# Kernel tuning notes

Hardware: AMD Instinct MI355X
Metric: run time of the kernel (lower is better)

## Reference

```python
import jax, jax.numpy as jnp
import numpy as np

B, S, D = 2, 4096, 256
H, DH, DM = 8, 32, 1024
ROPE_BASE = 10000.0
LN_EPS = 1e-5


def _layer_norm(x, g, b):
    mu = jnp.mean(x, axis=-1, keepdims=True)
    var = jnp.mean(jnp.square(x - mu), axis=-1, keepdims=True)
    return (x - mu) * jax.lax.rsqrt(var + LN_EPS) * g + b


def _rope(x):
    # x: [b, s, h, d_head]; lucidrains interleaved-pair RoPE
    s, d = x.shape[1], x.shape[-1]
    inv_freq = 1.0 / (ROPE_BASE ** (jnp.arange(0, d, 2, dtype=jnp.float32) / d))  # [d/2]
    freqs = jnp.arange(s, dtype=jnp.float32)[:, None] * inv_freq[None, :]          # [s, d/2]
    freqs = jnp.repeat(freqs, 2, axis=-1)                                          # [s, d]
    cos = jnp.cos(freqs)[None, :, None, :]
    sin = jnp.sin(freqs)[None, :, None, :]
    x1, x2 = x[..., 0::2], x[..., 1::2]
    rot = jnp.stack((-x2, x1), axis=-1).reshape(x.shape)
    return x * cos + rot * sin


def setup_inputs() -> dict:
    key = jax.random.key(0)
    ks = jax.random.split(key, 8)
    sw = 1.0 / np.sqrt(D)
    return {
        "x": jax.random.normal(ks[0], (B, S, D), jnp.float32),
        "Wq": jax.random.normal(ks[1], (D, D), jnp.float32) * sw,
        "Wk": jax.random.normal(ks[2], (D, D), jnp.float32) * sw,
        "Wv": jax.random.normal(ks[3], (D, D), jnp.float32) * sw,
        "Wo": jax.random.normal(ks[4], (D, D), jnp.float32) * sw,
        "ln1_g": jnp.ones((D,), jnp.float32),
        "ln1_b": jnp.zeros((D,), jnp.float32),
        "ln2_g": jnp.ones((D,), jnp.float32),
        "ln2_b": jnp.zeros((D,), jnp.float32),
        "W2": jax.random.normal(ks[5], (DM, D), jnp.float32) * sw,
        "b2": jnp.zeros((DM,), jnp.float32),
        "W3": jax.random.normal(ks[6], (D, DM), jnp.float32) * (1.0 / np.sqrt(DM)),
        "b3": jnp.zeros((D,), jnp.float32),
    }


def reference(x, Wq, Wk, Wv, Wo, ln1_g, ln1_b, ln2_g, ln2_b, W2, b2, W3, b3):
    b, s, d = x.shape
    h, dh = H, DH
    xn = _layer_norm(x, ln1_g, ln1_b)
    q = (xn @ Wq.T).reshape(b, s, h, dh)
    k = (xn @ Wk.T).reshape(b, s, h, dh)
    v = (xn @ Wv.T).reshape(b, s, h, dh)
    q = _rope(q)
    k = _rope(k)
    # scores: [b, h, q, k] (full matrix, matching original implementation)
    scores = jnp.einsum('bqhd,bkhd->bhqk', q, k) / np.sqrt(dh)
    attn = jax.nn.softmax(scores, axis=-1)
    out = jnp.einsum('bhqk,bkhd->bqhd', attn, v).reshape(b, s, d)
    out = out @ Wo.T
    mlp_in = out + x
    y = _layer_norm(mlp_in, ln2_g, ln2_b)
    y = jax.nn.gelu(y @ W2.T + b2, approximate=False)
    y = y @ W3.T + b3
    return y + mlp_in
```

## Files before the change

kernel.cpp:

```cpp
#include <hip/hip_runtime.h>
#include <math.h>

#define D 256
#define S 4096
#define H 8
#define DH 32
#define DM 1024
#define NTOK 8192

typedef __attribute__((ext_vector_type(8))) short short8;
typedef __attribute__((ext_vector_type(4))) float f32x4;

#define QSCALE (0.17677669529663687f * 1.4426950408889634f)

__device__ inline unsigned short f2bf(float f) {
    union { float f; unsigned u; } v; v.f = f;
    unsigned r = v.u + 0x7fffu + ((v.u >> 16) & 1u);
    return (unsigned short)(r >> 16);
}
__device__ inline void gload16(const void* g, void* l) {
    __builtin_amdgcn_global_load_lds((const __attribute__((address_space(1))) void*)g,
                                     (__attribute__((address_space(3))) void*)l, 16, 0, 0);
}

__device__ inline short8 pack_p(f32x4 s0, f32x4 s1) {
    unsigned u0[4], u1[4];
    #pragma unroll
    for (int i = 0; i < 4; ++i) {
        union { float f; unsigned u; } c0, c1;
        c0.f = __builtin_amdgcn_exp2f(s0[i]);
        c1.f = __builtin_amdgcn_exp2f(s1[i]);
        u0[i] = c0.u;
        u1[i] = c1.u;
    }
    union { unsigned u[4]; short8 s; } pk;
    pk.u[0] = __builtin_amdgcn_perm(u0[1], u0[0], 0x07060302u);
    pk.u[1] = __builtin_amdgcn_perm(u0[3], u0[2], 0x07060302u);
    pk.u[2] = __builtin_amdgcn_perm(u1[1], u1[0], 0x07060302u);
    pk.u[3] = __builtin_amdgcn_perm(u1[3], u1[2], 0x07060302u);
    return pk.s;
}

__global__ void prep(const float* __restrict__ Wq, const float* __restrict__ Wk,
                     const float* __restrict__ Wv, const float* __restrict__ Wo,
                     const float* __restrict__ W2, const float* __restrict__ W3,
                     unsigned short* __restrict__ wqkv, unsigned short* __restrict__ wo_b,
                     unsigned short* __restrict__ w2_b, unsigned short* __restrict__ w3_b,
                     float* __restrict__ ct, float* __restrict__ st,
                     const float* __restrict__ x, const float* __restrict__ g,
                     const float* __restrict__ b, unsigned short* __restrict__ xn) {
    int blk = blockIdx.x;
    if (blk < 3328) {
        int i = blk * 256 + threadIdx.x;
        if (i < 196608) {
            const float* s = (i < 65536) ? Wq : ((i < 131072) ? Wk : Wv);
            wqkv[i] = f2bf(s[i & 65535]);
        } else if (i < 262144) {
            wo_b[i - 196608] = f2bf(Wo[i - 196608]);
        } else if (i < 524288) {
            w2_b[i - 262144] = f2bf(W2[i - 262144]);
        } else if (i < 786432) {
            w3_b[i - 524288] = f2bf(W3[i - 524288]);
        } else {
            int j = i - 786432;
            int spos = j >> 4, pi = j & 15;
            float inv_freq = powf(10000.0f, -(float)(2 * pi) / 32.0f);
            float fr = (float)spos * inv_freq;
            ct[j] = cosf(fr);
            st[j] = sinf(fr);
        }
        return;
    }
    int l = threadIdx.x & 63;
    int row = (blk - 3328) * 4 + (threadIdx.x >> 6);
    const float4 v = *(const float4*)(x + (size_t)row * D + l * 4);
    float s  = v.x + v.y + v.z + v.w;
    float s2 = v.x * v.x + v.y * v.y + v.z * v.z + v.w * v.w;
    #pragma unroll
    for (int off = 32; off > 0; off >>= 1) {
        s  += __shfl_xor(s, off, 64);
        s2 += __shfl_xor(s2, off, 64);
    }
    float mu  = s * (1.0f / D);
    float var = s2 * (1.0f / D) - mu * mu;
    float rs  = rsqrtf(var + 1e-5f);
    const float4 gg = *(const float4*)(g + l * 4);
    const float4 bb = *(const float4*)(b + l * 4);
    ushort4 o;
    o.x = f2bf((v.x - mu) * rs * gg.x + bb.x);
    o.y = f2bf((v.y - mu) * rs * gg.y + bb.y);
    o.z = f2bf((v.z - mu) * rs * gg.z + bb.z);
    o.w = f2bf((v.w - mu) * rs * gg.w + bb.w);
    *(ushort4*)(xn + (size_t)row * D + l * 4) = o;
}

__global__ void ln_kernel(const float* __restrict__ x, const float* __restrict__ g,
                          const float* __restrict__ b, unsigned short* __restrict__ out) {
    int l = threadIdx.x & 63;
    int row = blockIdx.x * 4 + (threadIdx.x >> 6);
    const float4 v = *(const float4*)(x + (size_t)row * D + l * 4);
    float s  = v.x + v.y + v.z + v.w;
    float s2 = v.x * v.x + v.y * v.y + v.z * v.z + v.w * v.w;
    #pragma unroll
    for (int off = 32; off > 0; off >>= 1) {
        s  += __shfl_xor(s, off, 64);
        s2 += __shfl_xor(s2, off, 64);
    }
    float mu  = s * (1.0f / D);
    float var = s2 * (1.0f / D) - mu * mu;
    float rs  = rsqrtf(var + 1e-5f);
    const float4 gg = *(const float4*)(g + l * 4);
    const float4 bb = *(const float4*)(b + l * 4);
    ushort4 o;
    o.x = f2bf((v.x - mu) * rs * gg.x + bb.x);
    o.y = f2bf((v.y - mu) * rs * gg.y + bb.y);
    o.z = f2bf((v.z - mu) * rs * gg.z + bb.z);
    o.w = f2bf((v.w - mu) * rs * gg.w + bb.w);
    *(ushort4*)(out + (size_t)row * D + l * 4) = o;
}

__global__ __launch_bounds__(256) void gemm64b(const unsigned short* __restrict__ A,
        const unsigned short* __restrict__ Bw, void* __restrict__ outp,
        unsigned short* __restrict__ vt,
        const float* __restrict__ bias,
        const float* __restrict__ ct, const float* __restrict__ st,
        int N, int K, int mode) {
    __shared__ unsigned short As[2][64 * 64];
    __shared__ unsigned short Bs[2][64 * 64];
    int tid = threadIdx.x;
    int w = tid >> 6, l = tid & 63;
    int lm = l & 15, lg = l >> 4;
    int wm = (w >> 1) * 32, wn = (w & 1) * 32;
    int bm = blockIdx.x * 64, bn = blockIdx.y * 64;
    int r1 = tid >> 3, pc = tid & 7;
    int pcx = (pc ^ (r1 & 7)) * 8;
    const unsigned short* Ag1 = A + (size_t)(bm + r1) * K + pcx;
    const unsigned short* Ag2 = A + (size_t)(bm + 32 + r1) * K + pcx;
    const unsigned short* Bg1 = Bw + (size_t)(bn + r1) * K + pcx;
    const unsigned short* Bg2 = Bw + (size_t)(bn + 32 + r1) * K + pcx;
    const int swz = lm & 7;
    f32x4 acc[2][2] = {};

    gload16(Ag1, &As[0][w * 512]);
    gload16(Ag2, &As[0][2048 + w * 512]);
    gload16(Bg1, &Bs[0][w * 512]);
    gload16(Bg2, &Bs[0][2048 + w * 512]);
    for (int k0 = 0; k0 < K; k0 += 64) {
        int cur = (k0 >> 6) & 1;
        __syncthreads();
        if (k0 + 64 < K) {
            gload16(Ag1 + k0 + 64, &As[1 - cur][w * 512]);
            gload16(Ag2 + k0 + 64, &As[1 - cur][2048 + w * 512]);
            gload16(Bg1 + k0 + 64, &Bs[1 - cur][w * 512]);
            gload16(Bg2 + k0 + 64, &Bs[1 - cur][2048 + w * 512]);
        }
        #pragma unroll
        for (int j = 0; j < 2; ++j) {
            int ch = ((j * 4 + lg) ^ swz) * 8;
            short8 af[2], bf[2];
            #pragma unroll
            for (int i = 0; i < 2; ++i) af[i] = *(const short8*)&As[cur][(wm + i * 16 + lm) * 64 + ch];
            #pragma unroll
            for (int i = 0; i < 2; ++i) bf[i] = *(const short8*)&Bs[cur][(wn + i * 16 + lm) * 64 + ch];
            #pragma unroll
            for (int mi = 0; mi < 2; ++mi)
                #pragma unroll
                for (int ni = 0; ni < 2; ++ni)
                    acc[mi][ni] = __builtin_amdgcn_mfma_f32_16x16x32_bf16(af[mi], bf[ni], acc[mi][ni], 0, 0, 0);
        }
    }

    if (mode == 0) {
        if (bn >= 512) {
            #pragma unroll
            for (int mi = 0; mi < 2; ++mi) {
                #pragma unroll
                for (int ni = 0; ni < 2; ++ni) {
                    int ng = bn + wn + ni * 16 + lm - 512;
                    int hh = ng >> 5, dh = ng & 31;
                    int mg0 = bm + wm + mi * 16 + lg * 4;
                    int bb = mg0 >> 12, ss = mg0 & 4095;
                    ushort4 pv;
                    pv.x = f2bf(acc[mi][ni][0]); pv.y = f2bf(acc[mi][ni][1]);
                    pv.z = f2bf(acc[mi][ni][2]); pv.w = f2bf(acc[mi][ni][3]);
                    *(ushort4*)(vt + ((size_t)((bb * 8 + hh) * 32 + dh)) * S + ss) = pv;
                }
            }
        } else {
            #pragma unroll
            for (int mi = 0; mi < 2; ++mi) {
                #pragma unroll
                for (int ni = 0; ni < 2; ++ni) {
                    int ng = bn + wn + ni * 16 + lm;
                    int pi = (ng & 31) >> 1;
                    float sgn = (ng & 1) ? 1.f : -1.f;
                    float qs  = (ng < 256) ? QSCALE : 1.f;
                    #pragma unroll
                    for (int r2 = 0; r2 < 4; ++r2) {
                        int mg = bm + wm + mi * 16 + lg * 4 + r2;
                        int spos = mg & (S - 1);
                        float vv = acc[mi][ni][r2];
                        float pv = __shfl_xor(vv, 1, 64);
                        float cs = ct[spos * 16 + pi];
                        float sn = st[spos * 16 + pi];
                        float ov = (vv * cs + sgn * pv * sn) * qs;
                        ((unsigned short*)outp)[(size_t)mg * N + ng] = f2bf(ov);
                    }
                }
            }
        }
        return;
    }
    #pragma unroll
    for (int mi = 0; mi < 2; ++mi) {
        #pragma unroll
        for (int ni = 0; ni < 2; ++ni) {
            int ng = bn + wn + ni * 16 + lm;
            #pragma unroll
            for (int r2 = 0; r2 < 4; ++r2) {
                int mg = bm + wm + mi * 16 + lg * 4 + r2;
                float t = acc[mi][ni][r2] + bias[ng];
                ((unsigned short*)outp)[(size_t)mg * N + ng] =
                    f2bf(0.5f * t * (1.0f + erff(t * 0.70710678118654752f)));
            }
        }
    }
}

__global__ __launch_bounds__(256) void gemm32(const unsigned short* __restrict__ A,
        const unsigned short* __restrict__ Bw, void* __restrict__ outp,
        const float* __restrict__ bias, const float* __restrict__ res,
        int N, int K, int mode) {
    __shared__ unsigned short As[2][32 * 128];
    __shared__ unsigned short Bs[2][64 * 128];
    int tid = threadIdx.x;
    int w = tid >> 6, l = tid & 63;
    int lm = l & 15, lg = l >> 4;
    int rm = (w >> 1) * 16, wn = (w & 1) * 32;
    int bm = blockIdx.x * 32, bn = blockIdx.y * 64;
    int r1 = tid >> 4, pc = tid & 15;
    int pcx = (pc ^ (r1 & 7)) * 8;
    const unsigned short* Ag1 = A + (size_t)(bm + r1) * K + pcx;
    const unsigned short* Ag2 = A + (size_t)(bm + 16 + r1) * K + pcx;
    const unsigned short* Bg1 = Bw + (size_t)(bn + r1) * K + pcx;
    const unsigned short* Bg2 = Bw + (size_t)(bn + 16 + r1) * K + pcx;
    const unsigned short* Bg3 = Bw + (size_t)(bn + 32 + r1) * K + pcx;
    const unsigned short* Bg4 = Bw + (size_t)(bn + 48 + r1) * K + pcx;
    const int swz = lm & 7;
    f32x4 acc[2] = {};

    gload16(Ag1, &As[0][w * 512]);
    gload16(Ag2, &As[0][2048 + w * 512]);
    gload16(Bg1, &Bs[0][w * 512]);
    gload16(Bg2, &Bs[0][2048 + w * 512]);
    gload16(Bg3, &Bs[0][4096 + w * 512]);
    gload16(Bg4, &Bs[0][6144 + w * 512]);
    for (int k0 = 0; k0 < K; k0 += 128) {
        int cur = (k0 >> 7) & 1;
        __syncthreads();
        if (k0 + 128 < K) {
            gload16(Ag1 + k0 + 128, &As[1 - cur][w * 512]);
            gload16(Ag2 + k0 + 128, &As[1 - cur][2048 + w * 512]);
            gload16(Bg1 + k0 + 128, &Bs[1 - cur][w * 512]);
            gload16(Bg2 + k0 + 128, &Bs[1 - cur][2048 + w * 512]);
            gload16(Bg3 + k0 + 128, &Bs[1 - cur][4096 + w * 512]);
            gload16(Bg4 + k0 + 128, &Bs[1 - cur][6144 + w * 512]);
        }
        #pragma unroll
        for (int j = 0; j < 4; ++j) {
            int ch = ((j * 4 + lg) ^ swz) * 8;
            short8 af = *(const short8*)&As[cur][(rm + lm) * 128 + ch];
            short8 bf[2];
            #pragma unroll
            for (int i = 0; i < 2; ++i) bf[i] = *(const short8*)&Bs[cur][(wn + i * 16 + lm) * 128 + ch];
            #pragma unroll
            for (int ni = 0; ni < 2; ++ni)
                acc[ni] = __builtin_amdgcn_mfma_f32_16x16x32_bf16(af, bf[ni], acc[ni], 0, 0, 0);
        }
    }

    #pragma unroll
    for (int ni = 0; ni < 2; ++ni) {
        int ng = bn + wn + ni * 16 + lm;
        #pragma unroll
        for (int r2 = 0; r2 < 4; ++r2) {
            int mg = bm + rm + lg * 4 + r2;
            float v = acc[ni][r2];
            size_t idx = (size_t)mg * N + ng;
            if (mode == 1) {
                ((float*)outp)[idx] = v + res[idx];
            } else {
                ((float*)outp)[idx] = v + bias[ng] + res[idx];
            }
        }
    }
}

__global__ __launch_bounds__(512, 4) void attn_kernel(const unsigned short* __restrict__ Cq,
        const unsigned short* __restrict__ vt, unsigned short* __restrict__ out) {
    __shared__ unsigned short Ks[2][2][64][32];
    __shared__ unsigned short Vs[2][2][32][64];
    int tid = threadIdx.x;
    int w = tid >> 6, l = tid & 63;
    int grp = w >> 2, ws = w & 3;
    int lm = l & 15, lg = l >> 4;
    int qt = blockIdx.x >> 4;
    int bh = blockIdx.x & 15;
    int bb = bh >> 3, h = bh & 7;
    int q0 = qt * 128 + ws * 32;

    const short8 qfa = *(const short8*)(Cq + ((size_t)(bb * S + q0 + lm)) * 768 + h * DH + lg * 8);
    const short8 qfb = *(const short8*)(Cq + ((size_t)(bb * S + q0 + 16 + lm)) * 768 + h * DH + lg * 8);

    union { unsigned short us[8]; short8 s; } onesu;
    {
        unsigned short ov = (lm == 0) ? (unsigned short)0x3F80 : (unsigned short)0;
        #pragma unroll
        for (int i = 0; i < 8; ++i) onesu.us[i] = ov;
    }
    const short8 onef = onesu.s;

    int p = ws * 16 + (l >> 2);
    int krow = ((p >> 5) << 5) + (((p >> 2) & 3) << 3) + (((p >> 4) & 1) << 2) + (p & 3);
    const unsigned short* kg = Cq + ((size_t)(bb * S)) * 768 + 256 + h * 32
                               + (size_t)krow * 768 + ((l & 3) ^ ((l >> 3) & 3)) * 8;
    const unsigned short* vg = vt + ((size_t)(bh * 32 + ws * 8 + (l >> 3))) * S + ((l & 7) ^ (l >> 3)) * 8;
    const int kswz = (lm >> 1) & 3;
    const int vswz = lm & 7;

    f32x4 o0a = {0.f, 0.f, 0.f, 0.f}, o1a = {0.f, 0.f, 0.f, 0.f}, o2a = {0.f, 0.f, 0.f, 0.f};
    f32x4 o0b = {0.f, 0.f, 0.f, 0.f}, o1b = {0.f, 0.f, 0.f, 0.f}, o2b = {0.f, 0.f, 0.f, 0.f};
    const f32x4 z = {0.f, 0.f, 0.f, 0.f};

    gload16(kg + (size_t)grp * 64 * 768, &Ks[grp][0][ws * 16][0]);
    gload16(vg + (size_t)grp * 64,       &Vs[grp][0][ws * 8][0]);

    #pragma unroll 2
    for (int it = 0; it < S / 128; ++it) {
        int cur = it & 1;
        __syncthreads();
        if (it + 1 < S / 128) {
            size_t t = (size_t)(2 * (it + 1) + grp);
            gload16(kg + t * 64 * 768, &Ks[grp][1 - cur][ws * 16][0]);
            gload16(vg + t * 64,       &Vs[grp][1 - cur][ws * 8][0]);
        }
        #pragma unroll
        for (int half = 0; half < 2; ++half) {
            short8 kf0 = *(const short8*)&Ks[grp][cur][half * 32 + lm][(lg ^ kswz) * 8];
            short8 kf1 = *(const short8*)&Ks[grp][cur][half * 32 + 16 + lm][(lg ^ kswz) * 8];
            f32x4 s0a = __builtin_amdgcn_mfma_f32_16x16x32_bf16(kf0, qfa, z, 0, 0, 0);
            f32x4 s1a = __builtin_amdgcn_mfma_f32_16x16x32_bf16(kf1, qfa, z, 0, 0, 0);
            f32x4 s0b = __builtin_amdgcn_mfma_f32_16x16x32_bf16(kf0, qfb, z, 0, 0, 0);
            f32x4 s1b = __builtin_amdgcn_mfma_f32_16x16x32_bf16(kf1, qfb, z, 0, 0, 0);
            short8 pfa = pack_p(s0a, s1a);
            short8 pfb = pack_p(s0b, s1b);
            int vc = ((half * 4 + lg) ^ vswz) * 8;
            short8 va0 = *(const short8*)&Vs[grp][cur][lm][vc];
            short8 va1 = *(const short8*)&Vs[grp][cur][16 + lm][vc];
            o0a = __builtin_amdgcn_mfma_f32_16x16x32_bf16(va0, pfa, o0a, 0, 0, 0);
            o1a = __builtin_amdgcn_mfma_f32_16x16x32_bf16(va1, pfa, o1a, 0, 0, 0);
            o2a = __builtin_amdgcn_mfma_f32_16x16x32_bf16(onef, pfa, o2a, 0, 0, 0);
            o0b = __builtin_amdgcn_mfma_f32_16x16x32_bf16(va0, pfb, o0b, 0, 0, 0);
            o1b = __builtin_amdgcn_mfma_f32_16x16x32_bf16(va1, pfb, o1b, 0, 0, 0);
            o2b = __builtin_amdgcn_mfma_f32_16x16x32_bf16(onef, pfb, o2b, 0, 0, 0);
        }
    }
    f32x4* Red = (f32x4*)&Ks[0][0][0][0];
    float* Den = (float*)&Vs[0][0][0][0];
    __syncthreads();
    if (grp) {
        Red[(0 * 4 + ws) * 64 + l] = o0a;
        Red[(1 * 4 + ws) * 64 + l] = o1a;
        Red[(2 * 4 + ws) * 64 + l] = o0b;
        Red[(3 * 4 + ws) * 64 + l] = o1b;
        Den[(ws * 2 + 0) * 64 + l] = o2a[0];
        Den[(ws * 2 + 1) * 64 + l] = o2b[0];
    }
    __syncthreads();
    if (!grp) {
        f32x4 a0 = Red[(0 * 4 + ws) * 64 + l];
        f32x4 a1 = Red[(1 * 4 + ws) * 64 + l];
        f32x4 a2 = Red[(2 * 4 + ws) * 64 + l];
        f32x4 a3 = Red[(3 * 4 + ws) * 64 + l];
        float dda = o2a[0] + Den[(ws * 2 + 0) * 64 + l];
        float ddb = o2b[0] + Den[(ws * 2 + 1) * 64 + l];
        #pragma unroll
        for (int i = 0; i < 4; ++i) {
            o0a[i] += a0[i]; o1a[i] += a1[i];
            o0b[i] += a2[i]; o1b[i] += a3[i];
        }
        float inva = 1.0f / __shfl(dda, lm, 64);
        float invb = 1.0f / __shfl(ddb, lm, 64);
        ushort4 r0, r1;
        r0.x = f2bf(o0a[0] * inva); r0.y = f2bf(o0a[1] * inva);
        r0.z = f2bf(o0a[2] * inva); r0.w = f2bf(o0a[3] * inva);
        r1.x = f2bf(o1a[0] * inva); r1.y = f2bf(o1a[1] * inva);
        r1.z = f2bf(o1a[2] * inva); r1.w = f2bf(o1a[3] * inva);
        unsigned short* ob = out + ((size_t)(bb * S + q0 + lm)) * D + h * DH;
        *(ushort4*)(ob + lg * 4)      = r0;
        *(ushort4*)(ob + 16 + lg * 4) = r1;
        r0.x = f2bf(o0b[0] * invb); r0.y = f2bf(o0b[1] * invb);
        r0.z = f2bf(o0b[2] * invb); r0.w = f2bf(o0b[3] * invb);
        r1.x = f2bf(o1b[0] * invb); r1.y = f2bf(o1b[1] * invb);
        r1.z = f2bf(o1b[2] * invb); r1.w = f2bf(o1b[3] * invb);
        unsigned short* ob2 = out + ((size_t)(bb * S + q0 + 16 + lm)) * D + h * DH;
        *(ushort4*)(ob2 + lg * 4)      = r0;
        *(ushort4*)(ob2 + 16 + lg * 4) = r1;
    }
}

extern "C" void kernel_launch(void* const* d_in, const int* in_sizes, int n_in,
                              void* d_out, int out_size, void* d_ws, size_t ws_size,
                              hipStream_t stream) {
    const float* x     = (const float*)d_in[0];
    const float* Wq    = (const float*)d_in[1];
    const float* Wk    = (const float*)d_in[2];
    const float* Wv    = (const float*)d_in[3];
    const float* Wo    = (const float*)d_in[4];
    const float* ln1_g = (const float*)d_in[5];
    const float* ln1_b = (const float*)d_in[6];
    const float* ln2_g = (const float*)d_in[7];
    const float* ln2_b = (const float*)d_in[8];
    const float* W2    = (const float*)d_in[9];
    const float* b2    = (const float*)d_in[10];
    const float* W3    = (const float*)d_in[11];
    const float* b3    = (const float*)d_in[12];

    char* w8 = (char*)d_ws;
    unsigned short* wqkv = (unsigned short*)(w8);
    unsigned short* wo_b = (unsigned short*)(w8 + 393216);
    unsigned short* w2_b = (unsigned short*)(w8 + 524288);
    unsigned short* w3_b = (unsigned short*)(w8 + 1048576);
    float*          ct   = (float*)(w8 + 1572864);
    float*          st   = (float*)(w8 + 1835008);
    unsigned short* xn   = (unsigned short*)(w8 + 2097152);
    unsigned short* Cq   = (unsigned short*)(w8 + 6291456);
    unsigned short* hb   = Cq;
    unsigned short* vtb  = (unsigned short*)(w8 + 23068672);
    unsigned short* ab   = (unsigned short*)(w8 + 27262976);
    float*          mlpin= (float*)(w8 + 31457280);
    unsigned short* yn   = xn;

    prep<<<5376, 256, 0, stream>>>(Wq, Wk, Wv, Wo, W2, W3, wqkv, wo_b, w2_b, w3_b,
                                   ct, st, x, ln1_g, ln1_b, xn);
    gemm64b<<<dim3(128, 12), 256, 0, stream>>>(xn, wqkv, Cq, vtb, nullptr, ct, st, 768, 256, 0);
    attn_kernel<<<512, 512, 0, stream>>>(Cq, vtb, ab);
    gemm32<<<dim3(256, 4), 256, 0, stream>>>(ab, wo_b, mlpin, nullptr, x, 256, 256, 1);
    ln_kernel<<<NTOK / 4, 256, 0, stream>>>(mlpin, ln2_g, ln2_b, yn);
    gemm64b<<<dim3(128, 16), 256, 0, stream>>>(yn, w2_b, hb, nullptr, b2, nullptr, nullptr, 1024, 256, 2);
    gemm32<<<dim3(256, 4), 256, 0, stream>>>(hb, w3_b, (float*)d_out, b3, mlpin, 256, 1024, 3);
}
```

Baseline: 189.6 us.

## Triple-buffer attention K/V tiles with manual vmcnt waits and MFMA priority

Moves the attention kernel's K/V staging from a double buffer to a triple buffer, so loads are issued two tiles ahead. Waits are now explicit s_waitcnt vmcnt counts plus raw barriers instead of __syncthreads. setprio is raised around the MFMA groups so matrix work is favoured over other waves. This is meant to hide global-to-LDS latency better, at the cost of more LDS per block (which may lower occupancy) and redundant clamped loads in the last iterations.

```diff
diff --git a/kernel.cpp b/kernel.cpp
--- a/kernel.cpp
+++ b/kernel.cpp
@@ -298,8 +298,8 @@
 
 __global__ __launch_bounds__(512, 4) void attn_kernel(const unsigned short* __restrict__ Cq,
         const unsigned short* __restrict__ vt, unsigned short* __restrict__ out) {
-    __shared__ unsigned short Ks[2][2][64][32];
-    __shared__ unsigned short Vs[2][2][32][64];
+    __shared__ unsigned short Ks[2][3][64][32];
+    __shared__ unsigned short Vs[2][3][32][64];
     int tid = threadIdx.x;
     int w = tid >> 6, l = tid & 63;
     int grp = w >> 2, ws = w & 3;
@@ -332,39 +332,55 @@
     f32x4 o0b = {0.f, 0.f, 0.f, 0.f}, o1b = {0.f, 0.f, 0.f, 0.f}, o2b = {0.f, 0.f, 0.f, 0.f};
     const f32x4 z = {0.f, 0.f, 0.f, 0.f};
 
-    gload16(kg + (size_t)grp * 64 * 768, &Ks[grp][0][ws * 16][0]);
-    gload16(vg + (size_t)grp * 64,       &Vs[grp][0][ws * 8][0]);
-
-    #pragma unroll 2
-    for (int it = 0; it < S / 128; ++it) {
-        int cur = it & 1;
-        __syncthreads();
-        if (it + 1 < S / 128) {
-            size_t t = (size_t)(2 * (it + 1) + grp);
-            gload16(kg + t * 64 * 768, &Ks[grp][1 - cur][ws * 16][0]);
-            gload16(vg + t * 64,       &Vs[grp][1 - cur][ws * 8][0]);
-        }
-        #pragma unroll
-        for (int half = 0; half < 2; ++half) {
-            short8 kf0 = *(const short8*)&Ks[grp][cur][half * 32 + lm][(lg ^ kswz) * 8];
-            short8 kf1 = *(const short8*)&Ks[grp][cur][half * 32 + 16 + lm][(lg ^ kswz) * 8];
-            f32x4 s0a = __builtin_amdgcn_mfma_f32_16x16x32_bf16(kf0, qfa, z, 0, 0, 0);
-            f32x4 s1a = __builtin_amdgcn_mfma_f32_16x16x32_bf16(kf1, qfa, z, 0, 0, 0);
-            f32x4 s0b = __builtin_amdgcn_mfma_f32_16x16x32_bf16(kf0, qfb, z, 0, 0, 0);
-            f32x4 s1b = __builtin_amdgcn_mfma_f32_16x16x32_bf16(kf1, qfb, z, 0, 0, 0);
-            short8 pfa = pack_p(s0a, s1a);
-            short8 pfb = pack_p(s0b, s1b);
-            int vc = ((half * 4 + lg) ^ vswz) * 8;
-            short8 va0 = *(const short8*)&Vs[grp][cur][lm][vc];
-            short8 va1 = *(const short8*)&Vs[grp][cur][16 + lm][vc];
-            o0a = __builtin_amdgcn_mfma_f32_16x16x32_bf16(va0, pfa, o0a, 0, 0, 0);
-            o1a = __builtin_amdgcn_mfma_f32_16x16x32_bf16(va1, pfa, o1a, 0, 0, 0);
-            o2a = __builtin_amdgcn_mfma_f32_16x16x32_bf16(onef, pfa, o2a, 0, 0, 0);
-            o0b = __builtin_amdgcn_mfma_f32_16x16x32_bf16(va0, pfb, o0b, 0, 0, 0);
-            o1b = __builtin_amdgcn_mfma_f32_16x16x32_bf16(va1, pfb, o1b, 0, 0, 0);
-            o2b = __builtin_amdgcn_mfma_f32_16x16x32_bf16(onef, pfb, o2b, 0, 0, 0);
-        }
-    }
+    gload16(kg + (size_t)grp * 64 * 768,       &Ks[grp][0][ws * 16][0]);
+    gload16(vg + (size_t)grp * 64,             &Vs[grp][0][ws * 8][0]);
+    gload16(kg + (size_t)(2 + grp) * 64 * 768, &Ks[grp][1][ws * 16][0]);
+    gload16(vg + (size_t)(2 + grp) * 64,       &Vs[grp][1][ws * 8][0]);
+    asm volatile("s_waitcnt vmcnt(4)" ::: "memory");
+
+#define ATTN_STEP(J, CUR, NXT) do {                                                          \
+    asm volatile("s_waitcnt vmcnt(2) lgkmcnt(0)" ::: "memory");                              \
+    __builtin_amdgcn_s_barrier();                                                            \
+    __builtin_amdgcn_sched_barrier(0);                                                       \
+    int tt_ = (J) + 2; if (tt_ > 31) tt_ = 31;                                               \
+    size_t tg_ = (size_t)(2 * tt_ + grp);                                                    \
+    gload16(kg + tg_ * 64 * 768, &Ks[grp][NXT][ws * 16][0]);                                 \
+    gload16(vg + tg_ * 64,       &Vs[grp][NXT][ws * 8][0]);                                  \
+    _Pragma("unroll")                                                                        \
+    for (int half = 0; half < 2; ++half) {                                                   \
+        short8 kf0 = *(const short8*)&Ks[grp][CUR][half * 32 + lm][(lg ^ kswz) * 8];         \
+        short8 kf1 = *(const short8*)&Ks[grp][CUR][half * 32 + 16 + lm][(lg ^ kswz) * 8];    \
+        __builtin_amdgcn_s_setprio(1);                                                       \
+        f32x4 s0a = __builtin_amdgcn_mfma_f32_16x16x32_bf16(kf0, qfa, z, 0, 0, 0);           \
+        f32x4 s1a = __builtin_amdgcn_mfma_f32_16x16x32_bf16(kf1, qfa, z, 0, 0, 0);           \
+        f32x4 s0b = __builtin_amdgcn_mfma_f32_16x16x32_bf16(kf0, qfb, z, 0, 0, 0);           \
+        f32x4 s1b = __builtin_amdgcn_mfma_f32_16x16x32_bf16(kf1, qfb, z, 0, 0, 0);           \
+        __builtin_amdgcn_s_setprio(0);                                                       \
+        short8 pfa = pack_p(s0a, s1a);                                                       \
+        short8 pfb = pack_p(s0b, s1b);                                                       \
+        int vc = ((half * 4 + lg) ^ vswz) * 8;                                               \
+        short8 va0 = *(const short8*)&Vs[grp][CUR][lm][vc];                                  \
+        short8 va1 = *(const short8*)&Vs[grp][CUR][16 + lm][vc];                             \
+        __builtin_amdgcn_s_setprio(1);                                                       \
+        o0a = __builtin_amdgcn_mfma_f32_16x16x32_bf16(va0, pfa, o0a, 0, 0, 0);               \
+        o1a = __builtin_amdgcn_mfma_f32_16x16x32_bf16(va1, pfa, o1a, 0, 0, 0);               \
+        o2a = __builtin_amdgcn_mfma_f32_16x16x32_bf16(onef, pfa, o2a, 0, 0, 0);               \
+        o0b = __builtin_amdgcn_mfma_f32_16x16x32_bf16(va0, pfb, o0b, 0, 0, 0);               \
+        o1b = __builtin_amdgcn_mfma_f32_16x16x32_bf16(va1, pfb, o1b, 0, 0, 0);               \
+        o2b = __builtin_amdgcn_mfma_f32_16x16x32_bf16(onef, pfb, o2b, 0, 0, 0);               \
+        __builtin_amdgcn_s_setprio(0);                                                       \
+    }                                                                                        \
+} while (0)
+
+    for (int j3 = 0; j3 < 30; j3 += 3) {
+        ATTN_STEP(j3,     0, 2);
+        ATTN_STEP(j3 + 1, 1, 0);
+        ATTN_STEP(j3 + 2, 2, 1);
+    }
+    ATTN_STEP(30, 0, 2);
+    ATTN_STEP(31, 1, 0);
+#undef ATTN_STEP
+
     f32x4* Red = (f32x4*)&Ks[0][0][0][0];
     float* Den = (float*)&Vs[0][0][0][0];
     __syncthreads();
```

New measurement: 187.9 us. About the same (-0.9%).

## Load K/V fragments directly from global into registers, dropping LDS staging

Applied to the files above, without the earlier changes.

The attention kernel no longer stages K and V tiles through double-buffered shared memory with async global-to-LDS loads. Each wave now reads its MFMA operand fragments straight from global memory into registers, using a one-iteration register prefetch, an s_barrier per step, and s_setprio hints around the MFMA groups. This removes the LDS writes and reads and the __syncthreads per iteration. In exchange, every wave in a group fetches the same K/V data separately, which relies on cache hits and raises register pressure.

```diff
diff --git a/kernel.cpp b/kernel.cpp
--- a/kernel.cpp
+++ b/kernel.cpp
@@ -298,8 +298,8 @@
 
 __global__ __launch_bounds__(512, 4) void attn_kernel(const unsigned short* __restrict__ Cq,
         const unsigned short* __restrict__ vt, unsigned short* __restrict__ out) {
-    __shared__ unsigned short Ks[2][2][64][32];
-    __shared__ unsigned short Vs[2][2][32][64];
+    __shared__ f32x4 Red[16 * 64];
+    __shared__ float Den[8 * 64];
     int tid = threadIdx.x;
     int w = tid >> 6, l = tid & 63;
     int grp = w >> 2, ws = w & 3;
@@ -320,53 +320,78 @@
     }
     const short8 onef = onesu.s;
 
-    int p = ws * 16 + (l >> 2);
-    int krow = ((p >> 5) << 5) + (((p >> 2) & 3) << 3) + (((p >> 4) & 1) << 2) + (p & 3);
-    const unsigned short* kg = Cq + ((size_t)(bb * S)) * 768 + 256 + h * 32
-                               + (size_t)krow * 768 + ((l & 3) ^ ((l >> 3) & 3)) * 8;
-    const unsigned short* vg = vt + ((size_t)(bh * 32 + ws * 8 + (l >> 3))) * S + ((l & 7) ^ (l >> 3)) * 8;
-    const int kswz = (lm >> 1) & 3;
-    const int vswz = lm & 7;
+    int perm = ((lm >> 2) << 3) + (lm & 3);
+    const unsigned short* kb = Cq + ((size_t)(bb * S + grp * 64 + perm)) * 768
+                               + 256 + h * DH + lg * 8;
+    const unsigned short* vb = vt + ((size_t)(bh * 32 + lm)) * S + grp * 64 + lg * 8;
+    const size_t KSTEP = (size_t)128 * 768;
+    const size_t VSTEP = 128;
 
     f32x4 o0a = {0.f, 0.f, 0.f, 0.f}, o1a = {0.f, 0.f, 0.f, 0.f}, o2a = {0.f, 0.f, 0.f, 0.f};
     f32x4 o0b = {0.f, 0.f, 0.f, 0.f}, o1b = {0.f, 0.f, 0.f, 0.f}, o2b = {0.f, 0.f, 0.f, 0.f};
     const f32x4 z = {0.f, 0.f, 0.f, 0.f};
 
-    gload16(kg + (size_t)grp * 64 * 768, &Ks[grp][0][ws * 16][0]);
-    gload16(vg + (size_t)grp * 64,       &Vs[grp][0][ws * 8][0]);
+#define LD8(p) (*(const short8*)(p))
+    short8 k0 = LD8(kb);
+    short8 k1 = LD8(kb + 4 * 768);
+    short8 k2 = LD8(kb + 32 * 768);
+    short8 k3 = LD8(kb + 36 * 768);
+    short8 v0 = LD8(vb);
+    short8 v1 = LD8(vb + 16 * S);
+    short8 v2 = LD8(vb + 32);
+    short8 v3 = LD8(vb + 16 * S + 32);
 
     #pragma unroll 2
-    for (int it = 0; it < S / 128; ++it) {
-        int cur = it & 1;
-        __syncthreads();
-        if (it + 1 < S / 128) {
-            size_t t = (size_t)(2 * (it + 1) + grp);
-            gload16(kg + t * 64 * 768, &Ks[grp][1 - cur][ws * 16][0]);
-            gload16(vg + t * 64,       &Vs[grp][1 - cur][ws * 8][0]);
-        }
-        #pragma unroll
-        for (int half = 0; half < 2; ++half) {
-            short8 kf0 = *(const short8*)&Ks[grp][cur][half * 32 + lm][(lg ^ kswz) * 8];
-            short8 kf1 = *(const short8*)&Ks[grp][cur][half * 32 + 16 + lm][(lg ^ kswz) * 8];
-            f32x4 s0a = __builtin_amdgcn_mfma_f32_16x16x32_bf16(kf0, qfa, z, 0, 0, 0);
-            f32x4 s1a = __builtin_amdgcn_mfma_f32_16x16x32_bf16(kf1, qfa, z, 0, 0, 0);
-            f32x4 s0b = __builtin_amdgcn_mfma_f32_16x16x32_bf16(kf0, qfb, z, 0, 0, 0);
-            f32x4 s1b = __builtin_amdgcn_mfma_f32_16x16x32_bf16(kf1, qfb, z, 0, 0, 0);
-            short8 pfa = pack_p(s0a, s1a);
-            short8 pfb = pack_p(s0b, s1b);
-            int vc = ((half * 4 + lg) ^ vswz) * 8;
-            short8 va0 = *(const short8*)&Vs[grp][cur][lm][vc];
-            short8 va1 = *(const short8*)&Vs[grp][cur][16 + lm][vc];
-            o0a = __builtin_amdgcn_mfma_f32_16x16x32_bf16(va0, pfa, o0a, 0, 0, 0);
-            o1a = __builtin_amdgcn_mfma_f32_16x16x32_bf16(va1, pfa, o1a, 0, 0, 0);
-            o2a = __builtin_amdgcn_mfma_f32_16x16x32_bf16(onef, pfa, o2a, 0, 0, 0);
-            o0b = __builtin_amdgcn_mfma_f32_16x16x32_bf16(va0, pfb, o0b, 0, 0, 0);
-            o1b = __builtin_amdgcn_mfma_f32_16x16x32_bf16(va1, pfb, o1b, 0, 0, 0);
-            o2b = __builtin_amdgcn_mfma_f32_16x16x32_bf16(onef, pfb, o2b, 0, 0, 0);
-        }
-    }
-    f32x4* Red = (f32x4*)&Ks[0][0][0][0];
-    float* Den = (float*)&Vs[0][0][0][0];
+    for (int it = 0; it < 32; ++it) {
+        int tn = (it + 1 < 32) ? (it + 1) : it;
+        const unsigned short* kn = kb + (size_t)tn * KSTEP;
+        const unsigned short* vn = vb + (size_t)tn * VSTEP;
+        short8 nk0 = LD8(kn);
+        short8 nk1 = LD8(kn + 4 * 768);
+        short8 nk2 = LD8(kn + 32 * 768);
+        short8 nk3 = LD8(kn + 36 * 768);
+        __builtin_amdgcn_s_barrier();
+        __builtin_amdgcn_s_setprio(1);
+        f32x4 s0a = __builtin_amdgcn_mfma_f32_16x16x32_bf16(k0, qfa, z, 0, 0, 0);
+        f32x4 s1a = __builtin_amdgcn_mfma_f32_16x16x32_bf16(k1, qfa, z, 0, 0, 0);
+        f32x4 s0b = __builtin_amdgcn_mfma_f32_16x16x32_bf16(k0, qfb, z, 0, 0, 0);
+        f32x4 s1b = __builtin_amdgcn_mfma_f32_16x16x32_bf16(k1, qfb, z, 0, 0, 0);
+        __builtin_amdgcn_s_setprio(0);
+        short8 pfa = pack_p(s0a, s1a);
+        short8 pfb = pack_p(s0b, s1b);
+        __builtin_amdgcn_s_setprio(1);
+        o0a = __builtin_amdgcn_mfma_f32_16x16x32_bf16(v0, pfa, o0a, 0, 0, 0);
+        o1a = __builtin_amdgcn_mfma_f32_16x16x32_bf16(v1, pfa, o1a, 0, 0, 0);
+        o2a = __builtin_amdgcn_mfma_f32_16x16x32_bf16(onef, pfa, o2a, 0, 0, 0);
+        o0b = __builtin_amdgcn_mfma_f32_16x16x32_bf16(v0, pfb, o0b, 0, 0, 0);
+        o1b = __builtin_amdgcn_mfma_f32_16x16x32_bf16(v1, pfb, o1b, 0, 0, 0);
+        o2b = __builtin_amdgcn_mfma_f32_16x16x32_bf16(onef, pfb, o2b, 0, 0, 0);
+        __builtin_amdgcn_s_setprio(0);
+        short8 nv0 = LD8(vn);
+        short8 nv1 = LD8(vn + 16 * S);
+        short8 nv2 = LD8(vn + 32);
+        short8 nv3 = LD8(vn + 16 * S + 32);
+        __builtin_amdgcn_s_setprio(1);
+        f32x4 t0a = __builtin_amdgcn_mfma_f32_16x16x32_bf16(k2, qfa, z, 0, 0, 0);
+        f32x4 t1a = __builtin_amdgcn_mfma_f32_16x16x32_bf16(k3, qfa, z, 0, 0, 0);
+        f32x4 t0b = __builtin_amdgcn_mfma_f32_16x16x32_bf16(k2, qfb, z, 0, 0, 0);
+        f32x4 t1b = __builtin_amdgcn_mfma_f32_16x16x32_bf16(k3, qfb, z, 0, 0, 0);
+        __builtin_amdgcn_s_setprio(0);
+        short8 qfa2 = pack_p(t0a, t1a);
+        short8 qfb2 = pack_p(t0b, t1b);
+        __builtin_amdgcn_s_setprio(1);
+        o0a = __builtin_amdgcn_mfma_f32_16x16x32_bf16(v2, qfa2, o0a, 0, 0, 0);
+        o1a = __builtin_amdgcn_mfma_f32_16x16x32_bf16(v3, qfa2, o1a, 0, 0, 0);
+        o2a = __builtin_amdgcn_mfma_f32_16x16x32_bf16(onef, qfa2, o2a, 0, 0, 0);
+        o0b = __builtin_amdgcn_mfma_f32_16x16x32_bf16(v2, qfb2, o0b, 0, 0, 0);
+        o1b = __builtin_amdgcn_mfma_f32_16x16x32_bf16(v3, qfb2, o1b, 0, 0, 0);
+        o2b = __builtin_amdgcn_mfma_f32_16x16x32_bf16(onef, qfb2, o2b, 0, 0, 0);
+        __builtin_amdgcn_s_setprio(0);
+        k0 = nk0; k1 = nk1; k2 = nk2; k3 = nk3;
+        v0 = nv0; v1 = nv1; v2 = nv2; v3 = nv3;
+    }
+#undef LD8
+
     __syncthreads();
     if (grp) {
         Red[(0 * 4 + ws) * 64 + l] = o0a;
```

Measured after the change: 262.9 us. 38.7% more time.
